# Kernel tuning notes

Measured on AMD Instinct MI355X. Metric: run time of the kernel, lower is better.

## Reference

```python
import jax, jax.numpy as jnp
import numpy as np

N_ATOMS = 10000
N_EDGES = 500000
N_RADIAL = 5
N_BASIS = 7
N_SPECIES = 119
R_MIN = 0.5
R_MAX = 6.0
N_CONTR = 8
EMB_NORM = 1.0 / np.sqrt(N_BASIS)


def tril_2d_indices(n):
    return np.array([(i, j) for i in range(n) for j in range(i + 1)], dtype=np.int32)


def tril_3d_indices(n):
    return np.array([(i, j, k) for i in range(n) for j in range(i + 1) for k in range(j + 1)], dtype=np.int32)


TRI2 = tril_2d_indices(N_RADIAL)
TRI3 = tril_3d_indices(N_RADIAL)


def setup_inputs() -> dict:
    key = jax.random.key(0)
    k1, k2, k3, k4 = jax.random.split(key, 4)
    dr_vec = jax.random.normal(k1, (N_EDGES, 3), dtype=jnp.float32) * 1.5
    Z = jax.random.randint(k2, (N_ATOMS,), 0, N_SPECIES)
    neighbor_idxs = jax.random.randint(k3, (2, N_EDGES), 0, N_ATOMS)
    embeddings = jax.random.normal(k4, (N_SPECIES, N_SPECIES, N_RADIAL, N_BASIS), dtype=jnp.float32)
    return {"dr_vec": dr_vec, "Z": Z, "neighbor_idxs": neighbor_idxs, "embeddings": embeddings}


def _descriptor(dr_vec, embeddings, Z, neighbor_idxs):
    idx_i, idx_j = neighbor_idxs[0], neighbor_idxs[1]
    dr = jnp.linalg.norm(dr_vec, axis=-1)                      # [E]
    dn = dr_vec / (dr + 1e-5)[:, None]                         # [E,3] unit directions
    # --- radial function: Gaussian basis + species-pair coefficients + cosine cutoff ---
    betta = N_BASIS ** 2 / R_MAX ** 2
    rad_norm = (2.0 * betta / np.pi) ** 0.75
    shifts = (R_MIN + (R_MAX - R_MIN) / N_BASIS * np.arange(N_BASIS)).astype(np.float32)
    basis = rad_norm * jnp.exp(-betta * (dr[:, None] - shifts) ** 2)   # [E,B]
    coeffs = embeddings[Z[idx_i], Z[idx_j]]                            # [E,R,B] gather
    radial = jnp.einsum("erb,eb->er", coeffs, basis) * EMB_NORM        # [E,R]
    cutoff = 0.5 * (jnp.cos(np.pi * jnp.minimum(dr, R_MAX) / R_MAX) + 1.0)
    radial = radial * cutoff[:, None]
    # --- geometric moments: outer products of dn, scatter-added per atom ---
    xyz = dn[:, None, :]                                 # [E,1,3]
    m0 = radial                                          # [E,R]
    m1 = radial[..., None] * xyz                         # [E,R,3]
    m2 = m1[..., None] * xyz[:, :, None, :]              # [E,R,3,3]
    m3 = m2[..., None] * xyz[:, :, None, None, :]        # [E,R,3,3,3]
    seg = lambda x: jax.ops.segment_sum(x, idx_j, num_segments=N_ATOMS)
    M0, M1, M2, M3 = seg(m0), seg(m1), seg(m2), seg(m3)
    # --- triangular moment contractions into invariants ---
    c0 = M0
    c1 = jnp.einsum("ari,asi->ars", M1, M1)
    c2 = jnp.einsum("arij,asij->ars", M2, M2)
    c3 = jnp.einsum("arijk,asijk->ars", M3, M3)
    c4 = jnp.einsum("arij,asik,atjk->arst", M2, M2, M2)
    c5 = jnp.einsum("ari,asj,atij->arst", M1, M1, M2)
    c6 = jnp.einsum("arijk,asijl,atkl->arst", M3, M3, M2)
    c7 = jnp.einsum("arijk,asij,atk->arst", M3, M2, M1)
    i2, j2 = TRI2[:, 0], TRI2[:, 1]
    i3, j3, k3 = TRI3[:, 0], TRI3[:, 1], TRI3[:, 2]
    n_atoms = c0.shape[0]
    c1 = c1[:, i2, j2]
    c2 = c2[:, i2, j2]
    c3 = c3[:, i2, j2]
    c4 = c4[:, i3, j3, k3]
    c5 = c5[:, i2, j2].reshape(n_atoms, -1)   # symmetric in (r,s)
    c6 = c6[:, i2, j2].reshape(n_atoms, -1)   # symmetric in (r,s)
    c7 = c7.reshape(n_atoms, -1)              # no symmetry
    feats = [c0, c1, c2, c3, c4, c5, c6, c7][:N_CONTR]
    return jnp.concatenate(feats, axis=-1)    # [n_atoms, 360]


def reference(dr_vec, Z, neighbor_idxs, embeddings):
    return _descriptor(dr_vec, embeddings, Z, neighbor_idxs)
```

## Files before the change

### kernel.cpp

```cpp
#include <hip/hip_runtime.h>
#include <cmath>

#define NSPEC 119
#define FEAT 360
#define CAP 128
#define G 16
#define NPAIR (NSPEC*NSPEC*35)

__global__ __launch_bounds__(256) void gm_prep_kernel(
    const float* __restrict__ emb, float* __restrict__ emb_pad,
    int* __restrict__ cnt, int n_atoms)
{
    int t = blockIdx.x * 256 + threadIdx.x;
    if (t < NPAIR) {
        int p = t / 35;
        int b = t - p * 35;
        emb_pad[36 * p + b] = emb[t];
    }
    if (t < n_atoms) cnt[t] = 0;
}

__global__ __launch_bounds__(256) void gm_scatter_kernel(
    const float* __restrict__ dr_vec,
    const int* __restrict__ Z,
    const int* __restrict__ nbr,
    const float* __restrict__ emb_pad,
    int* __restrict__ cnt,
    float* __restrict__ bucket,
    int n_edges, float rad_norm)
{
    int e = blockIdx.x * 256 + threadIdx.x;
    if (e >= n_edges) return;
    float x = dr_vec[3*e+0];
    float y = dr_vec[3*e+1];
    float z = dr_vec[3*e+2];
    int ai = nbr[e];
    int aj = nbr[n_edges + e];
    int Zi = Z[ai], Zj = Z[aj];

    const float4* cp = (const float4*)(emb_pad + (size_t)(Zi*NSPEC + Zj) * 36);
    float co[36];
#pragma unroll
    for (int q = 0; q < 9; ++q) {
        float4 v = cp[q];
        co[4*q+0] = v.x; co[4*q+1] = v.y; co[4*q+2] = v.z; co[4*q+3] = v.w;
    }

    float dr = sqrtf(x*x + y*y + z*z);
    float inv = 1.0f / (dr + 1e-5f);
    float dx = x*inv, dy = y*inv, dz = z*inv;

    const float betta = 49.0f/36.0f;
    float basis[7];
#pragma unroll
    for (int b = 0; b < 7; ++b) {
        float t = dr - (0.5f + (5.5f/7.0f)*(float)b);
        basis[b] = rad_norm * __expf(-betta*t*t);
    }
    float cutoff = 0.5f * (__cosf(fminf(dr, 6.0f) * 0.52359877559829887f) + 1.0f);
    float sc = cutoff * 0.37796447300922720f;

    float rad[5];
#pragma unroll
    for (int r = 0; r < 5; ++r) {
        float acc = 0.0f;
#pragma unroll
        for (int b = 0; b < 7; ++b) acc = fmaf(co[r*7+b], basis[b], acc);
        rad[r] = acc * sc;
    }

    int pos = atomicAdd(&cnt[aj], 1);
    if (pos < CAP) {
        float4* rec = (float4*)(bucket + ((size_t)aj * CAP + pos) * 8);
        rec[0] = make_float4(rad[0], rad[1], rad[2], rad[3]);
        rec[1] = make_float4(rad[4], dx, dy, dz);
    }
}

__global__ __launch_bounds__(256) void gm_accum_kernel(
    const int* __restrict__ cnt,
    const float* __restrict__ bucket,
    float* __restrict__ out,
    int n_atoms)
{
    __shared__ float MS[16][100];
    int tid = blockIdx.x * 256 + threadIdx.x;
    int a  = tid / G;
    int sl = tid & (G-1);
    int la = threadIdx.x >> 4;
    if (a >= n_atoms) return;

    int c = cnt[a]; if (c > CAP) c = CAP;

    float m[100];
#pragma unroll
    for (int i = 0; i < 100; ++i) m[i] = 0.f;

    for (int k = sl; k < c; k += G) {
        const float4* rec = (const float4*)(bucket + ((size_t)a * CAP + k) * 8);
        float4 r0 = rec[0];
        float4 r1 = rec[1];
        float rad[5] = {r0.x, r0.y, r0.z, r0.w, r1.x};
        float dx = r1.y, dy = r1.z, dz = r1.w;

        float p2[6] = {dx*dx, dx*dy, dx*dz, dy*dy, dy*dz, dz*dz};
        float p3[10] = {p2[0]*dx, p2[0]*dy, p2[0]*dz,
                        p2[3]*dx, p2[4]*dx, p2[5]*dx,
                        p2[3]*dy, p2[3]*dz,
                        p2[4]*dz, p2[5]*dz};

#pragma unroll
        for (int r = 0; r < 5; ++r) {
            float v = rad[r];
            m[r] += v;
            m[5 + r*3 + 0] = fmaf(v, dx, m[5 + r*3 + 0]);
            m[5 + r*3 + 1] = fmaf(v, dy, m[5 + r*3 + 1]);
            m[5 + r*3 + 2] = fmaf(v, dz, m[5 + r*3 + 2]);
#pragma unroll
            for (int u = 0; u < 6; ++u)
                m[20 + r*6 + u] = fmaf(v, p2[u], m[20 + r*6 + u]);
#pragma unroll
            for (int u = 0; u < 10; ++u)
                m[50 + r*10 + u] = fmaf(v, p3[u], m[50 + r*10 + u]);
        }
    }

#pragma unroll
    for (int i = 0; i < 100; ++i) {
        m[i] += __shfl_xor(m[i], 1, 64);
        m[i] += __shfl_xor(m[i], 2, 64);
        m[i] += __shfl_xor(m[i], 4, 64);
        m[i] += __shfl_xor(m[i], 8, 64);
    }

    if (sl == 0) {
#pragma unroll
        for (int i = 0; i < 100; ++i) MS[la][i] = m[i];
    }

    float* F = out + (size_t)a * FEAT;
    const float* S = &MS[la][0];

    const int S2[3][3] = {{0,1,2},{1,3,4},{2,4,5}};
    const int S3[3][3][3] = {
        {{0,1,2},{1,3,4},{2,4,5}},
        {{1,3,4},{3,6,7},{4,7,8}},
        {{2,4,5},{4,7,8},{5,8,9}}};
    const float w6[6]   = {1,2,2,1,2,1};
    const float w10[10] = {1,3,3,3,6,3,1,3,3,1};
    const int   PI[6] = {0,0,0,1,1,2};
    const int   PJ[6] = {0,1,2,1,2,2};
    const float PW[6] = {1,2,2,1,2,1};

    if (sl < 5) F[sl] = S[sl];

    int p = sl;
    if (p < 15) {
        int r = (p >= 10) ? 4 : ((p >= 6) ? 3 : ((p >= 3) ? 2 : ((p >= 1) ? 1 : 0)));
        int s = p - (r*(r+1))/2;
        const float* M1r = S + 5  + 3*r;
        const float* M1s = S + 5  + 3*s;
        const float* M2r = S + 20 + 6*r;
        const float* M2s = S + 20 + 6*s;
        const float* M3r = S + 50 + 10*r;
        const float* M3s = S + 50 + 10*s;
        float m1r[3], m1s[3], m2r[6], m2s[6], m3r[10], m3s[10];
#pragma unroll
        for (int i = 0; i < 3; ++i)  { m1r[i] = M1r[i]; m1s[i] = M1s[i]; }
#pragma unroll
        for (int u = 0; u < 6; ++u)  { m2r[u] = M2r[u]; m2s[u] = M2s[u]; }
#pragma unroll
        for (int u = 0; u < 10; ++u) { m3r[u] = M3r[u]; m3s[u] = M3s[u]; }

        float a1 = 0.f, a2 = 0.f, a3 = 0.f;
#pragma unroll
        for (int i = 0; i < 3; ++i)  a1 = fmaf(m1r[i], m1s[i], a1);
#pragma unroll
        for (int u = 0; u < 6; ++u)  a2 = fmaf(w6[u]*m2r[u],  m2s[u], a2);
#pragma unroll
        for (int u = 0; u < 10; ++u) a3 = fmaf(w10[u]*m3r[u], m3s[u], a3);
        F[5 + p]  = a1;
        F[20 + p] = a2;
        F[35 + p] = a3;

        float P[3][3];
#pragma unroll
        for (int j = 0; j < 3; ++j)
#pragma unroll
        for (int k = 0; k < 3; ++k) {
            float acc = 0.f;
#pragma unroll
            for (int i = 0; i < 3; ++i)
                acc = fmaf(m2r[S2[i][j]], m2s[S2[i][k]], acc);
            P[j][k] = acc;
        }
        float PA[6] = {P[0][0], P[0][1]+P[1][0], P[0][2]+P[2][0],
                       P[1][1], P[1][2]+P[2][1], P[2][2]};
        int qb = (r*(r+1)*(r+2))/6 + (s*(s+1))/2;
        for (int t = 0; t <= s; ++t) {
            const float* M2t = S + 20 + 6*t;
            float acc = 0.f;
#pragma unroll
            for (int u = 0; u < 6; ++u) acc = fmaf(PA[u], M2t[u], acc);
            F[50 + qb + t] = acc;
        }

        float A[6] = {m1r[0]*m1s[0],
                      m1r[0]*m1s[1] + m1r[1]*m1s[0],
                      m1r[0]*m1s[2] + m1r[2]*m1s[0],
                      m1r[1]*m1s[1],
                      m1r[1]*m1s[2] + m1r[2]*m1s[1],
                      m1r[2]*m1s[2]};
#pragma unroll
        for (int t = 0; t < 5; ++t) {
            const float* M2t = S + 20 + 6*t;
            float acc = 0.f;
#pragma unroll
            for (int u = 0; u < 6; ++u) acc = fmaf(A[u], M2t[u], acc);
            F[85 + p*5 + t] = acc;
        }

        float Q[3][3];
#pragma unroll
        for (int k = 0; k < 3; ++k)
#pragma unroll
        for (int l = 0; l < 3; ++l) {
            float acc = 0.f;
#pragma unroll
            for (int u = 0; u < 6; ++u)
                acc = fmaf(PW[u]*m3r[S3[PI[u]][PJ[u]][k]],
                           m3s[S3[PI[u]][PJ[u]][l]], acc);
            Q[k][l] = acc;
        }
        float QA[6] = {Q[0][0], Q[0][1]+Q[1][0], Q[0][2]+Q[2][0],
                       Q[1][1], Q[1][2]+Q[2][1], Q[2][2]};
#pragma unroll
        for (int t = 0; t < 5; ++t) {
            const float* M2t = S + 20 + 6*t;
            float acc = 0.f;
#pragma unroll
            for (int u = 0; u < 6; ++u) acc = fmaf(QA[u], M2t[u], acc);
            F[160 + p*5 + t] = acc;
        }
    }

#pragma unroll
    for (int hh = 0; hh < 2; ++hh) {
        int h = sl + 16*hh;
        if (h < 25) {
            int r = h / 5;
            int s = h - 5*r;
            const float* M3r = S + 50 + 10*r;
            const float* M2s = S + 20 + 6*s;
            float m3r[10], m2s[6];
#pragma unroll
            for (int u = 0; u < 10; ++u) m3r[u] = M3r[u];
#pragma unroll
            for (int u = 0; u < 6; ++u)  m2s[u] = M2s[u];
            float B[3];
#pragma unroll
            for (int k = 0; k < 3; ++k) {
                float acc = 0.f;
#pragma unroll
                for (int u = 0; u < 6; ++u)
                    acc = fmaf(PW[u]*m3r[S3[PI[u]][PJ[u]][k]], m2s[u], acc);
                B[k] = acc;
            }
#pragma unroll
            for (int t = 0; t < 5; ++t) {
                const float* M1t = S + 5 + 3*t;
                F[235 + r*25 + s*5 + t] =
                    fmaf(B[0], M1t[0], fmaf(B[1], M1t[1], B[2]*M1t[2]));
            }
        }
    }
}

extern "C" void kernel_launch(void* const* d_in, const int* in_sizes, int n_in,
                              void* d_out, int out_size, void* d_ws, size_t ws_size,
                              hipStream_t stream) {
    const float* dr_vec = (const float*)d_in[0];
    const int*   Z      = (const int*)d_in[1];
    const int*   nbr    = (const int*)d_in[2];
    const float* emb    = (const float*)d_in[3];
    float* out = (float*)d_out;

    int n_edges = in_sizes[0] / 3;
    int n_atoms = in_sizes[1];

    int*   cnt     = (int*)d_ws;
    float* emb_pad = (float*)((char*)d_ws + 65536);
    float* bucket  = (float*)((char*)d_ws + 2104832);

    float rad_norm = (float)pow(2.0 * (49.0/36.0) / M_PI, 0.75);

    int prep_n = (NPAIR > n_atoms) ? NPAIR : n_atoms;
    gm_prep_kernel<<<(prep_n + 255)/256, 256, 0, stream>>>(emb, emb_pad, cnt, n_atoms);

    gm_scatter_kernel<<<(n_edges + 255)/256, 256, 0, stream>>>(
        dr_vec, Z, nbr, emb_pad, cnt, bucket, n_edges, rad_norm);

    int accum_threads = n_atoms * G;
    gm_accum_kernel<<<(accum_threads + 255)/256, 256, 0, stream>>>(
        cnt, bucket, out, n_atoms);
}
```

Baseline: 138.9 us.

## Store embeddings as fp16, byte species, padded counters, issue atomic early

The prep kernel now converts the species-pair embedding table to half precision with 64-element rows and packs Z into bytes. This shrinks the gather footprint in the scatter kernel, which now loads five 16-byte vectors per edge instead of nine. Per-atom counters are padded to 64-byte spacing to reduce atomic contention on shared cache lines, and the atomicAdd is issued before the math so its latency can overlap. Rounding the coefficients to fp16 introduces error in the radial values that may matter against the reference tolerance.

```diff
diff --git a/kernel.cpp b/kernel.cpp
--- a/kernel.cpp
+++ b/kernel.cpp
@@ -1,4 +1,5 @@
 #include <hip/hip_runtime.h>
+#include <hip/hip_fp16.h>
 #include <cmath>
 
 #define NSPEC 119
@@ -6,44 +7,60 @@
 #define CAP 128
 #define G 16
 #define NPAIR (NSPEC*NSPEC*35)
+#define CNTSTRIDE 16
 
 __global__ __launch_bounds__(256) void gm_prep_kernel(
-    const float* __restrict__ emb, float* __restrict__ emb_pad,
+    const float* __restrict__ emb, __half* __restrict__ emb_h,
+    const int* __restrict__ Z, unsigned char* __restrict__ Zb,
     int* __restrict__ cnt, int n_atoms)
 {
     int t = blockIdx.x * 256 + threadIdx.x;
     if (t < NPAIR) {
         int p = t / 35;
         int b = t - p * 35;
-        emb_pad[36 * p + b] = emb[t];
-    }
-    if (t < n_atoms) cnt[t] = 0;
+        emb_h[(p << 6) + b] = __float2half_rn(emb[t]);
+    }
+    if (t < n_atoms) {
+        Zb[t] = (unsigned char)Z[t];
+        cnt[t * CNTSTRIDE] = 0;
+    }
 }
 
 __global__ __launch_bounds__(256) void gm_scatter_kernel(
     const float* __restrict__ dr_vec,
-    const int* __restrict__ Z,
+    const unsigned char* __restrict__ Zb,
     const int* __restrict__ nbr,
-    const float* __restrict__ emb_pad,
+    const __half* __restrict__ emb_h,
     int* __restrict__ cnt,
     float* __restrict__ bucket,
     int n_edges, float rad_norm)
 {
     int e = blockIdx.x * 256 + threadIdx.x;
     if (e >= n_edges) return;
+
+    int ai = nbr[e];
+    int aj = nbr[n_edges + e];
+    int pos = atomicAdd(&cnt[aj * CNTSTRIDE], 1);
+
     float x = dr_vec[3*e+0];
     float y = dr_vec[3*e+1];
     float z = dr_vec[3*e+2];
-    int ai = nbr[e];
-    int aj = nbr[n_edges + e];
-    int Zi = Z[ai], Zj = Z[aj];
-
-    const float4* cp = (const float4*)(emb_pad + (size_t)(Zi*NSPEC + Zj) * 36);
+    int Zi = Zb[ai], Zj = Zb[aj];
+
+    const uint4* p4 = (const uint4*)(emb_h + ((size_t)(Zi*NSPEC + Zj) << 6));
+    uint buf[20];
+    *(uint4*)(buf +  0) = p4[0];
+    *(uint4*)(buf +  4) = p4[1];
+    *(uint4*)(buf +  8) = p4[2];
+    *(uint4*)(buf + 12) = p4[3];
+    *(uint4*)(buf + 16) = p4[4];
+    const __half2* hb = (const __half2*)buf;
     float co[36];
 #pragma unroll
-    for (int q = 0; q < 9; ++q) {
-        float4 v = cp[q];
-        co[4*q+0] = v.x; co[4*q+1] = v.y; co[4*q+2] = v.z; co[4*q+3] = v.w;
+    for (int k = 0; k < 18; ++k) {
+        float2 f = __half22float2(hb[k]);
+        co[2*k]   = f.x;
+        co[2*k+1] = f.y;
     }
 
     float dr = sqrtf(x*x + y*y + z*z);
@@ -69,7 +86,6 @@
         rad[r] = acc * sc;
     }
 
-    int pos = atomicAdd(&cnt[aj], 1);
     if (pos < CAP) {
         float4* rec = (float4*)(bucket + ((size_t)aj * CAP + pos) * 8);
         rec[0] = make_float4(rad[0], rad[1], rad[2], rad[3]);
@@ -90,7 +106,7 @@
     int la = threadIdx.x >> 4;
     if (a >= n_atoms) return;
 
-    int c = cnt[a]; if (c > CAP) c = CAP;
+    int c = cnt[a * CNTSTRIDE]; if (c > CAP) c = CAP;
 
     float m[100];
 #pragma unroll
@@ -288,17 +304,18 @@
     int n_edges = in_sizes[0] / 3;
     int n_atoms = in_sizes[1];
 
-    int*   cnt     = (int*)d_ws;
-    float* emb_pad = (float*)((char*)d_ws + 65536);
-    float* bucket  = (float*)((char*)d_ws + 2104832);
+    int*           cnt   = (int*)d_ws;
+    unsigned char* Zb    = (unsigned char*)((char*)d_ws + 655360);
+    __half*        emb_h = (__half*)((char*)d_ws + 665600);
+    float*         bucket= (float*)((char*)d_ws + 2478208);
 
     float rad_norm = (float)pow(2.0 * (49.0/36.0) / M_PI, 0.75);
 
     int prep_n = (NPAIR > n_atoms) ? NPAIR : n_atoms;
-    gm_prep_kernel<<<(prep_n + 255)/256, 256, 0, stream>>>(emb, emb_pad, cnt, n_atoms);
+    gm_prep_kernel<<<(prep_n + 255)/256, 256, 0, stream>>>(emb, emb_h, Z, Zb, cnt, n_atoms);
 
     gm_scatter_kernel<<<(n_edges + 255)/256, 256, 0, stream>>>(
-        dr_vec, Z, nbr, emb_pad, cnt, bucket, n_edges, rad_norm);
+        dr_vec, Zb, nbr, emb_h, cnt, bucket, n_edges, rad_norm);
 
     int accum_threads = n_atoms * G;
     gm_accum_kernel<<<(accum_threads + 255)/256, 256, 0, stream>>>(
```

New measurement: 124.0 us. 10.7% less time.
